# Performance work log

Hardware: AMD Instinct MI355X
Metric: run time of the kernel (lower is better)

The kernel has to match this reference:

```python
import jax, jax.numpy as jnp
import numpy as np
from jax import lax

# Orthonormal 2x2 Haar (db1). Analysis uses dwt_scale per coefficient; the
# synthesis uses 0.5*idwt_scale so that dwt_scale=0.5, idwt_scale=1.0 gives a
# perfect round trip (Hadamard matrix M, M@M = 4I, M symmetric).
DWT_SCALE = 0.5
IDWT_SCALE = 1.0
WT_LEVELS = 3
STRIDE = 1
PAD = 1  # (kernel_size - 1) // 2


def dwt2(x, s):
    # x: (B, C, H, W) -> (B, C, 4, H/2, W/2), subband order LL, LH, HL, HH
    a = x[..., 0::2, 0::2]
    b = x[..., 0::2, 1::2]
    c = x[..., 1::2, 0::2]
    d = x[..., 1::2, 1::2]
    ll = (a + b + c + d) * s
    lh = (a - b + c - d) * s
    hl = (a + b - c - d) * s
    hh = (a - b - c + d) * s
    return jnp.stack([ll, lh, hl, hh], axis=2)


def idwt2(sub, s):
    # sub: (B, C, 4, h, w) -> (B, C, 2h, 2w); inverse of dwt2 when s = 0.5/ (4*dwt_s) * ... here Hadamard symmetric
    ll, lh, hl, hh = sub[:, :, 0], sub[:, :, 1], sub[:, :, 2], sub[:, :, 3]
    a = (ll + lh + hl + hh) * s
    b = (ll - lh + hl - hh) * s
    c = (ll + lh - hl - hh) * s
    d = (ll - lh - hl + hh) * s
    B, C, h, w = a.shape
    row0 = jnp.stack([a, b], axis=-1).reshape(B, C, h, 2 * w)
    row1 = jnp.stack([c, d], axis=-1).reshape(B, C, h, 2 * w)
    return jnp.stack([row0, row1], axis=-2).reshape(B, C, 2 * h, 2 * w)


def conv2d(x, w, stride, pad):
    return lax.conv_general_dilated(
        x, w, window_strides=(stride, stride),
        padding=[(pad, pad), (pad, pad)],
        dimension_numbers=('NCHW', 'OIHW', 'NCHW'))


def wtconv_core(x, weight):
    cout4 = weight.shape[0]
    cout = cout4 // 4
    curr_ll = x
    ll_levels, high_levels = [], []
    for _ in range(WT_LEVELS):
        sub = dwt2(curr_ll, DWT_SCALE)             # (B, C, 4, h, w)
        B, C, _, h, w = sub.shape
        y = conv2d(sub.reshape(B, C * 4, h, w), weight, STRIDE, PAD)
        y = y.reshape(B, cout, 4, h, w)
        ll_levels.append(y[:, :, 0])
        high_levels.append(y[:, :, 1:])
        curr_ll = sub[:, :, 0]                     # pre-conv LL feeds next level
    next_ll = jnp.zeros_like(ll_levels[-1])
    for ll, hi in zip(reversed(ll_levels), reversed(high_levels)):
        ll = ll + next_ll
        sub = jnp.concatenate([ll[:, :, None], hi], axis=2)
        next_ll = idwt2(sub, 0.5 * IDWT_SCALE)
    return next_ll


def setup_inputs() -> dict:
    key = jax.random.key(0)
    k1, k2, k3 = jax.random.split(key, 3)
    B, C, H, W = 8, 32, 224, 224
    K = 3
    x = jax.random.normal(k1, (B, C, H, W), dtype=jnp.float32)
    fan_in = C * 4 * K * K
    bound = np.sqrt(6.0 / ((1.0 + 2.236 ** 2) * fan_in))
    weight = jax.random.uniform(k2, (C * 4, C * 4, K, K), dtype=jnp.float32,
                                minval=-bound, maxval=bound)
    bias = jax.random.normal(k3, (C,), dtype=jnp.float32) * 0.01
    return {"x": x, "weight": weight, "bias": bias}


def reference(x, weight, bias):
    H, W = x.shape[-2:]
    pad_factor = 2 ** WT_LEVELS
    pad_h = (pad_factor - H % pad_factor) % pad_factor
    pad_w = (pad_factor - W % pad_factor) % pad_factor
    xp = x
    if pad_h > 0 or pad_w > 0:
        xp = jnp.pad(x, ((0, 0), (0, 0), (0, pad_h), (0, pad_w)), mode='reflect')
    out = wtconv_core(xp, weight)
    out = out[..., :H, :W]
    return out + bias[None, :, None, None]
```

## Files before the change

kernel.cpp:

```cpp
#include <hip/hip_runtime.h>

typedef __bf16 bf16_t;
typedef __bf16 bf16x4_t __attribute__((ext_vector_type(4)));
typedef __bf16 bf16x8_t __attribute__((ext_vector_type(8)));
typedef float f32x16_t __attribute__((ext_vector_type(16)));

__device__ __forceinline__ void repack_body(const float* __restrict__ w,
                                            bf16_t* __restrict__ wt2,
                                            int o) {
  int e = o & 7;
  int lane = (o >> 3) & 63;
  int f = o >> 9;
  int wc = f & 1;
  int nt = (f >> 1) & 1;
  int kc = (f >> 2) & 3;
  int hk = (f >> 4) & 1;
  int t = f >> 5;
  int oc = wc * 64 + nt * 32 + (lane & 31);
  int ic = (hk * 8 + kc * 2 + (lane >> 5)) * 8 + e;
  wt2[o] = (bf16_t)w[((size_t)oc * 128 + ic) * 9 + t];
}

__device__ __forceinline__ void dwt_body(const float* __restrict__ in,
                                         bf16_t* __restrict__ sub,
                                         float* __restrict__ llout,
                                         int h, int w, bf16_t* lds) {
  const int bi = blockIdx.z;
  const int i = blockIdx.y;
  const int j0 = blockIdx.x * 64;
  const int tid = threadIdx.x;
  const int j = tid & 63;
  const int cg = tid >> 6;
  const int jg = j0 + j;
  const bool jok = jg < w;
  const int H2 = h * 2, W2 = w * 2;
  for (int c = cg; c < 32; c += 4) {
    float va = 0.f, vb = 0.f, vc = 0.f, vd = 0.f;
    if (jok) {
      const float2* p0 = (const float2*)(in + ((size_t)(bi * 32 + c) * H2 + 2 * i) * W2);
      const float2* p1 = (const float2*)(in + ((size_t)(bi * 32 + c) * H2 + 2 * i + 1) * W2);
      float2 r0 = p0[jg];
      float2 r1 = p1[jg];
      va = r0.x; vb = r0.y; vc = r1.x; vd = r1.y;
    }
    float ll = (va + vb + vc + vd) * 0.5f;
    float lh = (va - vb + vc - vd) * 0.5f;
    float hl = (va + vb - vc - vd) * 0.5f;
    float hh = (va - vb - vc + vd) * 0.5f;
    bf16x4_t q;
    q.x = (bf16_t)ll; q.y = (bf16_t)lh; q.z = (bf16_t)hl; q.w = (bf16_t)hh;
    *(bf16x4_t*)(&lds[j * 132 + c * 4]) = q;
    if (llout != nullptr && jok)
      llout[((size_t)(bi * 32 + c) * h + i) * w + jg] = ll;
  }
  __syncthreads();
  const size_t obase = ((size_t)bi * h + i) * w;
  for (int it = 0; it < 8; ++it) {
    int flat = it * 256 + tid;
    int jj = flat >> 5;
    int c4 = flat & 31;
    if (j0 + jj < w) {
      bf16x4_t q = *(const bf16x4_t*)(&lds[jj * 132 + c4 * 4]);
      *(bf16x4_t*)(sub + ((obase + j0 + jj) << 7) + c4 * 4) = q;
    }
  }
}

__global__ __launch_bounds__(256) void dwt0_kernel(const float* __restrict__ in,
                                                   bf16_t* __restrict__ sub,
                                                   float* __restrict__ llout,
                                                   const float* __restrict__ wsrc,
                                                   bf16_t* __restrict__ wt2,
                                                   int h, int w) {
  __shared__ __align__(16) bf16_t lds[64 * 132];
  if (blockIdx.z == 8) {
    int bid = blockIdx.y * 2 + blockIdx.x;
    for (int o = bid * 256 + threadIdx.x; o < 147456; o += 224 * 256)
      repack_body(wsrc, wt2, o);
    return;
  }
  dwt_body(in, sub, llout, h, w, lds);
}

__global__ __launch_bounds__(256) void dwt_kernel(const float* __restrict__ in,
                                                  bf16_t* __restrict__ sub,
                                                  float* __restrict__ llout,
                                                  int h, int w) {
  __shared__ __align__(16) bf16_t lds[64 * 132];
  dwt_body(in, sub, llout, h, w, lds);
}

__device__ __forceinline__ void conv_idwt_tile(
    const bf16_t* __restrict__ sub, const bf16_t* __restrict__ wt2,
    const float* __restrict__ nll, const float* __restrict__ nllup,
    const float* __restrict__ bias, float* __restrict__ out,
    int h, int w, int bi, int y0, int x0, int och, uint4* smemV) {
  char* haloS = (char*)smemV;
  float* scr = (float*)((char*)smemV + 23040);
  const int tid = threadIdx.x;
  const size_t img_base = (size_t)bi * h * w;

  const int lane = tid & 63;
  const int wav = tid >> 6;
  const int m = lane & 31;
  const int hw_ = lane >> 5;
  const int il = wav * 2 + (m >> 4);
  const int jl = m & 15;
  const int pixA = il * 18 + jl;
  const bf16_t* wlane = wt2 + (lane << 3) + (och << 9);

  f32x16_t acc[2] = {};

  for (int hk = 0; hk < 2; ++hk) {
    if (hk) __syncthreads();
    for (int it = 0; it < 6; ++it) {
      int flat = it * 256 + tid;
      int pix = flat >> 3;
      int ch = flat & 7;
      if (pix < 180) {
        int r = pix / 18;
        int c = pix - r * 18;
        int gy = y0 + r - 1;
        int gx = x0 + c - 1;
        uint4 v = make_uint4(0u, 0u, 0u, 0u);
        if ((unsigned)gy < (unsigned)h && (unsigned)gx < (unsigned)w)
          v = *(const uint4*)(sub + ((img_base + (size_t)gy * w + gx) << 7) +
                              ((hk * 8 + ch) << 3));
        *(uint4*)(haloS + (pix << 7) + ((ch ^ (pix & 7)) << 4)) = v;
      }
    }
    __syncthreads();

#pragma unroll
    for (int t = 0; t < 9; ++t) {
      const int ky = t / 3;
      const int kx = t - ky * 3;
      const bf16_t* wb = wlane + ((t * 2 + hk) << 13);
      bf16x8_t bfrag[4][2];
#pragma unroll
      for (int kc = 0; kc < 4; ++kc) {
        bfrag[kc][0] = *(const bf16x8_t*)(wb + (kc << 11));
        bfrag[kc][1] = *(const bf16x8_t*)(wb + (kc << 11) + 1024);
      }
      const int pix0 = pixA + ky * 18 + kx;
      const int s0 = pix0 & 7;
      const char* hp0 = haloS + (pix0 << 7);
#pragma unroll
      for (int kc = 0; kc < 4; ++kc) {
        const int cidx = kc * 2 + hw_;
        bf16x8_t a0 = *(const bf16x8_t*)(hp0 + ((cidx ^ s0) << 4));
        acc[0] = __builtin_amdgcn_mfma_f32_32x32x16_bf16(a0, bfrag[kc][0], acc[0], 0, 0, 0);
        acc[1] = __builtin_amdgcn_mfma_f32_32x32x16_bf16(a0, bfrag[kc][1], acc[1], 0, 0, 0);
      }
    }
  }

  const int W2 = w * 2;
  const int H2 = h * 2;
  const int hu = h >> 1, wu = w >> 1;
  const int mh_t = m >> 4;
  const int mm = m & 15;
  const int kw = mm >> 2;
  const int sw = mm & 3;

#pragma unroll
  for (int ph = 0; ph < 4; ++ph) {
    const int nt = ph >> 1;
    const int mh = ph & 1;
    if (ph) __syncthreads();
    if (mh_t == mh) {
#pragma unroll
      for (int reg = 0; reg < 16; ++reg) {
        int row = (reg & 3) + ((reg >> 2) << 3) + (hw_ << 2);
        int px = wav * 32 + row;
        scr[px * 17 + (kw << 2) + sw] = acc[nt][reg];
      }
    }
    __syncthreads();
#pragma unroll
    for (int it = 0; it < 2; ++it) {
      int idx = it * 256 + tid;
      int ox4 = idx & 7;
      int dy = (idx >> 3) & 1;
      int row = (idx >> 4) & 7;
      int k = (idx >> 7) & 3;
      int gy = y0 + row;
      int gx = x0 + ox4 * 2;
      if (gy >= h || gx >= w) continue;
      int p0 = row * 16 + ox4 * 2;
      int p1 = p0 + 1;
      float4 sa = *(const float4*)(&scr[p0 * 17 + (k << 2)]);
      float4 sb = *(const float4*)(&scr[p1 * 17 + (k << 2)]);
      float sg = dy ? -1.f : 1.f;
      float e0 = sa.x + sa.y + sg * (sa.z + sa.w);
      float e1 = sa.x - sa.y + sg * (sa.z - sa.w);
      float e2 = sb.x + sb.y + sg * (sb.z + sb.w);
      float e3 = sb.x - sb.y + sg * (sb.z - sb.w);
      int ch = och * 16 + nt * 8 + mh * 4 + k;
      float n0 = 0.f, n1 = 0.f;
      if (nll != nullptr) {
        const float* np = nll + ((size_t)(bi * 32 + ch) * h + gy) * w + gx;
        float2 nv = *(const float2*)np;
        n0 = nv.x; n1 = nv.y;
      }
      if (nllup != nullptr) {
        float u = nllup[((size_t)(bi * 32 + ch) * hu + (gy >> 1)) * wu + (gx >> 1)];
        n0 += 0.5f * u;
        n1 += 0.5f * u;
      }
      float bv = (bias != nullptr) ? bias[ch] : 0.f;
      float4 o;
      o.x = 0.5f * e0 + 0.5f * n0 + bv;
      o.y = 0.5f * e1 + 0.5f * n0 + bv;
      o.z = 0.5f * e2 + 0.5f * n1 + bv;
      o.w = 0.5f * e3 + 0.5f * n1 + bv;
      float* op = out + ((size_t)(bi * 32 + ch) * H2 + 2 * gy + dy) * W2 + 2 * gx;
      *(float4*)op = o;
    }
  }
}

__global__ __launch_bounds__(256, 4) void conv_idwt_kernel(
    const bf16_t* __restrict__ sub, const bf16_t* __restrict__ wt2,
    const float* __restrict__ nll, const float* __restrict__ nllup,
    const float* __restrict__ bias, float* __restrict__ out, int h, int w) {
  __shared__ uint4 smemV[1984];
  conv_idwt_tile(sub, wt2, nll, nllup, bias, out, h, w,
                 blockIdx.z, blockIdx.y * 8, (blockIdx.x >> 1) * 16,
                 blockIdx.x & 1, smemV);
}

__global__ __launch_bounds__(256, 4) void conv12_kernel(
    const bf16_t* __restrict__ sub1, const bf16_t* __restrict__ sub2,
    const bf16_t* __restrict__ wt2, float* __restrict__ nll1raw,
    float* __restrict__ nll2) {
  __shared__ uint4 smemV[1984];
  const int B = blockIdx.x;
  const bf16_t* sub;
  float* outp;
  int hh, bi, by, bx, och;
  if (B < 448) {
    och = B & 1;
    int q = B >> 1;
    bx = q & 3;
    int r = q >> 2;
    by = r % 7;
    bi = r / 7;
    sub = sub1; outp = nll1raw; hh = 56;
  } else {
    int lb = B - 448;
    och = lb & 1;
    int q = lb >> 1;
    bx = q & 1;
    int r = q >> 1;
    by = r & 3;
    bi = r >> 2;
    sub = sub2; outp = nll2; hh = 28;
  }
  conv_idwt_tile(sub, wt2, nullptr, nullptr, nullptr, outp, hh, hh,
                 bi, by * 8, bx * 16, och, smemV);
}

extern "C" void kernel_launch(void* const* d_in, const int* in_sizes, int n_in,
                              void* d_out, int out_size, void* d_ws, size_t ws_size,
                              hipStream_t stream) {
  if (ws_size < 66125824u) return;

  const float* x = (const float*)d_in[0];
  const float* weight = (const float*)d_in[1];
  const float* bias = (const float*)d_in[2];
  float* out = (float*)d_out;
  char* ws = (char*)d_ws;

  bf16_t* wt2 = (bf16_t*)(ws);
  bf16_t* sub0 = (bf16_t*)(ws + 294912);
  bf16_t* sub1 = (bf16_t*)(ws + 25985024);
  bf16_t* sub2 = (bf16_t*)(ws + 32407552);
  float* ll0 = (float*)(ws + 34013184);
  float* ll1 = (float*)(ws + 46858240);
  float* nll2 = (float*)(ws + 50069504);
  float* nll1 = (float*)(ws + 53280768);

  dwt0_kernel<<<dim3(2, 112, 9), 256, 0, stream>>>(x, sub0, ll0, weight, wt2, 112, 112);
  dwt_kernel<<<dim3(1, 56, 8), 256, 0, stream>>>(ll0, sub1, ll1, 56, 56);
  dwt_kernel<<<dim3(1, 28, 8), 256, 0, stream>>>(ll1, sub2, nullptr, 28, 28);
  conv12_kernel<<<576, 256, 0, stream>>>(sub1, sub2, wt2, nll1, nll2);
  conv_idwt_kernel<<<dim3(14, 14, 8), 256, 0, stream>>>(sub0, wt2, nll1, nll2, bias, out, 112, 112);
}
```

Baseline: 216.0 us.

## Retile conv so each wave owns an output-channel half over a 4x16 tile

The conv tile moves from 256 threads (8x16 pixels, with the two output-channel halves in separate blocks) to 128 threads (4x16 pixels). Each of the two waves now handles one output-channel half and two M-tiles of pixels, so one shared halo load serves all 128 output channels. This removes the duplicated halo loads across the two channel-half blocks and doubles the MFMAs per loaded weight fragment. In exchange there are more blocks, a smaller halo with proportionally more overlap rows, more accumulator registers, and occupancy set by the new launch bounds.

Result: slower. 254.9 us (+18.0%).

```diff
diff --git a/kernel.cpp b/kernel.cpp
--- a/kernel.cpp
+++ b/kernel.cpp
@@ -94,30 +94,30 @@
     const bf16_t* __restrict__ sub, const bf16_t* __restrict__ wt2,
     const float* __restrict__ nll, const float* __restrict__ nllup,
     const float* __restrict__ bias, float* __restrict__ out,
-    int h, int w, int bi, int y0, int x0, int och, uint4* smemV) {
+    int h, int w, int bi, int y0, int x0, uint4* smemV) {
   char* haloS = (char*)smemV;
-  float* scr = (float*)((char*)smemV + 23040);
+  float* scr = (float*)((char*)smemV + 13824);
   const int tid = threadIdx.x;
   const size_t img_base = (size_t)bi * h * w;
 
   const int lane = tid & 63;
-  const int wav = tid >> 6;
+  const int och = tid >> 6;
   const int m = lane & 31;
   const int hw_ = lane >> 5;
-  const int il = wav * 2 + (m >> 4);
+  const int il = m >> 4;
   const int jl = m & 15;
   const int pixA = il * 18 + jl;
   const bf16_t* wlane = wt2 + (lane << 3) + (och << 9);
 
-  f32x16_t acc[2] = {};
+  f32x16_t acc[2][2] = {};
 
   for (int hk = 0; hk < 2; ++hk) {
     if (hk) __syncthreads();
-    for (int it = 0; it < 6; ++it) {
-      int flat = it * 256 + tid;
+    for (int it = 0; it < 7; ++it) {
+      int flat = it * 128 + tid;
       int pix = flat >> 3;
       int ch = flat & 7;
-      if (pix < 180) {
+      if (pix < 108) {
         int r = pix / 18;
         int c = pix - r * 18;
         int gy = y0 + r - 1;
@@ -143,14 +143,20 @@
         bfrag[kc][1] = *(const bf16x8_t*)(wb + (kc << 11) + 1024);
       }
       const int pix0 = pixA + ky * 18 + kx;
+      const int pix1 = pix0 + 36;
       const int s0 = pix0 & 7;
+      const int s1 = pix1 & 7;
       const char* hp0 = haloS + (pix0 << 7);
+      const char* hp1 = haloS + (pix1 << 7);
 #pragma unroll
       for (int kc = 0; kc < 4; ++kc) {
         const int cidx = kc * 2 + hw_;
         bf16x8_t a0 = *(const bf16x8_t*)(hp0 + ((cidx ^ s0) << 4));
-        acc[0] = __builtin_amdgcn_mfma_f32_32x32x16_bf16(a0, bfrag[kc][0], acc[0], 0, 0, 0);
-        acc[1] = __builtin_amdgcn_mfma_f32_32x32x16_bf16(a0, bfrag[kc][1], acc[1], 0, 0, 0);
+        bf16x8_t a1 = *(const bf16x8_t*)(hp1 + ((cidx ^ s1) << 4));
+        acc[0][0] = __builtin_amdgcn_mfma_f32_32x32x16_bf16(a0, bfrag[kc][0], acc[0][0], 0, 0, 0);
+        acc[0][1] = __builtin_amdgcn_mfma_f32_32x32x16_bf16(a0, bfrag[kc][1], acc[0][1], 0, 0, 0);
+        acc[1][0] = __builtin_amdgcn_mfma_f32_32x32x16_bf16(a1, bfrag[kc][0], acc[1][0], 0, 0, 0);
+        acc[1][1] = __builtin_amdgcn_mfma_f32_32x32x16_bf16(a1, bfrag[kc][1], acc[1][1], 0, 0, 0);
       }
     }
   }
@@ -160,8 +166,6 @@
   const int hu = h >> 1, wu = w >> 1;
   const int mh_t = m >> 4;
   const int mm = m & 15;
-  const int kw = mm >> 2;
-  const int sw = mm & 3;
 
 #pragma unroll
   for (int ph = 0; ph < 4; ++ph) {
@@ -170,33 +174,36 @@
     if (ph) __syncthreads();
     if (mh_t == mh) {
 #pragma unroll
-      for (int reg = 0; reg < 16; ++reg) {
-        int row = (reg & 3) + ((reg >> 2) << 3) + (hw_ << 2);
-        int px = wav * 32 + row;
-        scr[px * 17 + (kw << 2) + sw] = acc[nt][reg];
+      for (int mt = 0; mt < 2; ++mt) {
+#pragma unroll
+        for (int reg = 0; reg < 16; ++reg) {
+          int row = (reg & 3) + ((reg >> 2) << 3) + (hw_ << 2);
+          int px = mt * 32 + row;
+          scr[px * 33 + (och << 4) + mm] = acc[mt][nt][reg];
+        }
       }
     }
     __syncthreads();
 #pragma unroll
-    for (int it = 0; it < 2; ++it) {
-      int idx = it * 256 + tid;
+    for (int it = 0; it < 4; ++it) {
+      int idx = it * 128 + tid;
       int ox4 = idx & 7;
       int dy = (idx >> 3) & 1;
-      int row = (idx >> 4) & 7;
-      int k = (idx >> 7) & 3;
+      int row = (idx >> 4) & 3;
+      int chl = idx >> 6;
       int gy = y0 + row;
       int gx = x0 + ox4 * 2;
       if (gy >= h || gx >= w) continue;
-      int p0 = row * 16 + ox4 * 2;
+      int p0 = ((row >> 1) << 5) + ((row & 1) << 4) + (ox4 << 1);
       int p1 = p0 + 1;
-      float4 sa = *(const float4*)(&scr[p0 * 17 + (k << 2)]);
-      float4 sb = *(const float4*)(&scr[p1 * 17 + (k << 2)]);
+      float4 sa = *(const float4*)(&scr[p0 * 33 + (chl << 2)]);
+      float4 sb = *(const float4*)(&scr[p1 * 33 + (chl << 2)]);
       float sg = dy ? -1.f : 1.f;
       float e0 = sa.x + sa.y + sg * (sa.z + sa.w);
       float e1 = sa.x - sa.y + sg * (sa.z - sa.w);
       float e2 = sb.x + sb.y + sg * (sb.z + sb.w);
       float e3 = sb.x - sb.y + sg * (sb.z - sb.w);
-      int ch = och * 16 + nt * 8 + mh * 4 + k;
+      int ch = ((chl >> 2) << 4) + nt * 8 + mh * 4 + (chl & 3);
       float n0 = 0.f, n1 = 0.f;
       if (nll != nullptr) {
         const float* np = nll + ((size_t)(bi * 32 + ch) * h + gy) * w + gx;
@@ -220,45 +227,40 @@
   }
 }
 
-__global__ __launch_bounds__(256, 4) void conv_idwt_kernel(
+__global__ __launch_bounds__(128, 3) void conv_idwt_kernel(
     const bf16_t* __restrict__ sub, const bf16_t* __restrict__ wt2,
     const float* __restrict__ nll, const float* __restrict__ nllup,
     const float* __restrict__ bias, float* __restrict__ out, int h, int w) {
-  __shared__ uint4 smemV[1984];
+  __shared__ uint4 smemV[1392];
   conv_idwt_tile(sub, wt2, nll, nllup, bias, out, h, w,
-                 blockIdx.z, blockIdx.y * 8, (blockIdx.x >> 1) * 16,
-                 blockIdx.x & 1, smemV);
-}
-
-__global__ __launch_bounds__(256, 4) void conv12_kernel(
+                 blockIdx.z, blockIdx.y * 4, blockIdx.x * 16, smemV);
+}
+
+__global__ __launch_bounds__(128, 3) void conv12_kernel(
     const bf16_t* __restrict__ sub1, const bf16_t* __restrict__ sub2,
     const bf16_t* __restrict__ wt2, float* __restrict__ nll1raw,
     float* __restrict__ nll2) {
-  __shared__ uint4 smemV[1984];
+  __shared__ uint4 smemV[1392];
   const int B = blockIdx.x;
   const bf16_t* sub;
   float* outp;
-  int hh, bi, by, bx, och;
+  int hh, bi, by, bx;
   if (B < 448) {
-    och = B & 1;
-    int q = B >> 1;
-    bx = q & 3;
-    int r = q >> 2;
-    by = r % 7;
-    bi = r / 7;
+    bx = B & 3;
+    int r = B >> 2;
+    by = r % 14;
+    bi = r / 14;
     sub = sub1; outp = nll1raw; hh = 56;
   } else {
     int lb = B - 448;
-    och = lb & 1;
-    int q = lb >> 1;
-    bx = q & 1;
-    int r = q >> 1;
-    by = r & 3;
-    bi = r >> 2;
+    bx = lb & 1;
+    int r = lb >> 1;
+    by = r % 7;
+    bi = r / 7;
     sub = sub2; outp = nll2; hh = 28;
   }
   conv_idwt_tile(sub, wt2, nullptr, nullptr, nullptr, outp, hh, hh,
-                 bi, by * 8, bx * 16, och, smemV);
+                 bi, by * 4, bx * 16, smemV);
 }
 
 extern "C" void kernel_launch(void* const* d_in, const int* in_sizes, int n_in,
@@ -284,6 +286,6 @@
   dwt0_kernel<<<dim3(2, 112, 9), 256, 0, stream>>>(x, sub0, ll0, weight, wt2, 112, 112);
   dwt_kernel<<<dim3(1, 56, 8), 256, 0, stream>>>(ll0, sub1, ll1, 56, 56);
   dwt_kernel<<<dim3(1, 28, 8), 256, 0, stream>>>(ll1, sub2, nullptr, 28, 28);
-  conv12_kernel<<<576, 256, 0, stream>>>(sub1, sub2, wt2, nll1, nll2);
-  conv_idwt_kernel<<<dim3(14, 14, 8), 256, 0, stream>>>(sub0, wt2, nll1, nll2, bias, out, 112, 112);
-}
+  conv12_kernel<<<560, 128, 0, stream>>>(sub1, sub2, wt2, nll1, nll2);
+  conv_idwt_kernel<<<dim3(7, 28, 8), 128, 0, stream>>>(sub0, wt2, nll1, nll2, bias, out, 112, 112);
+}
```

## Stage conv weights through double-buffered LDS via async global_load_lds

Applied to the files above, without the earlier changes.

Weight fragments were previously loaded from global memory into registers by every wave for each tap. They are now copied cooperatively into a double-buffered LDS region with global_load_lds, prefetching the next tap while the current tap's MFMAs run. This cuts redundant global weight traffic and register pressure. In exchange it adds a vmcnt drain and a block barrier per tap and grows LDS per block, which may lower occupancy.

Measured after the change: 188.0 us. -13.0%, faster.

```diff
diff --git a/kernel.cpp b/kernel.cpp
--- a/kernel.cpp
+++ b/kernel.cpp
@@ -4,6 +4,10 @@
 typedef __bf16 bf16x4_t __attribute__((ext_vector_type(4)));
 typedef __bf16 bf16x8_t __attribute__((ext_vector_type(8)));
 typedef float f32x16_t __attribute__((ext_vector_type(16)));
+
+#define AS_G(p) ((const __attribute__((address_space(1))) void*)(p))
+#define AS_L(p) ((__attribute__((address_space(3))) void*)(p))
+#define DRAIN_VM() asm volatile("s_waitcnt vmcnt(0)" ::: "memory")
 
 __device__ __forceinline__ void repack_body(const float* __restrict__ w,
                                             bf16_t* __restrict__ wt2,
@@ -96,18 +100,18 @@
     const float* __restrict__ bias, float* __restrict__ out,
     int h, int w, int bi, int y0, int x0, int och, uint4* smemV) {
   char* haloS = (char*)smemV;
+  char* Bbuf = (char*)smemV + 23040;
   float* scr = (float*)((char*)smemV + 23040);
   const int tid = threadIdx.x;
   const size_t img_base = (size_t)bi * h * w;
 
   const int lane = tid & 63;
-  const int wav = tid >> 6;
+  const int wv = tid >> 6;
   const int m = lane & 31;
   const int hw_ = lane >> 5;
-  const int il = wav * 2 + (m >> 4);
+  const int il = wv * 2 + (m >> 4);
   const int jl = m & 15;
   const int pixA = il * 18 + jl;
-  const bf16_t* wlane = wt2 + (lane << 3) + (och << 9);
 
   f32x16_t acc[2] = {};
 
@@ -129,29 +133,47 @@
         *(uint4*)(haloS + (pix << 7) + ((ch ^ (pix & 7)) << 4)) = v;
       }
     }
+    {
+      const int th0 = hk;
+#pragma unroll
+      for (int q = 0; q < 2; ++q) {
+        const bf16_t* srcp = wt2 + (((th0 << 4) + (wv << 2) + (q << 1) + och) << 9) + (lane << 3);
+        __builtin_amdgcn_global_load_lds(AS_G(srcp),
+            AS_L(Bbuf + (((wv << 1) + q) << 10)), 16, 0, 0);
+      }
+    }
+    DRAIN_VM();
     __syncthreads();
 
-#pragma unroll
+    int cur = 0;
     for (int t = 0; t < 9; ++t) {
+      if (t < 8) {
+        const int thn = ((t + 1) << 1) + hk;
+#pragma unroll
+        for (int q = 0; q < 2; ++q) {
+          const bf16_t* srcp = wt2 + (((thn << 4) + (wv << 2) + (q << 1) + och) << 9) + (lane << 3);
+          __builtin_amdgcn_global_load_lds(AS_G(srcp),
+              AS_L(Bbuf + ((cur ^ 1) << 13) + (((wv << 1) + q) << 10)), 16, 0, 0);
+        }
+      }
       const int ky = t / 3;
       const int kx = t - ky * 3;
-      const bf16_t* wb = wlane + ((t * 2 + hk) << 13);
-      bf16x8_t bfrag[4][2];
-#pragma unroll
-      for (int kc = 0; kc < 4; ++kc) {
-        bfrag[kc][0] = *(const bf16x8_t*)(wb + (kc << 11));
-        bfrag[kc][1] = *(const bf16x8_t*)(wb + (kc << 11) + 1024);
-      }
       const int pix0 = pixA + ky * 18 + kx;
       const int s0 = pix0 & 7;
       const char* hp0 = haloS + (pix0 << 7);
+      const char* bp = Bbuf + (cur << 13) + (lane << 4);
 #pragma unroll
       for (int kc = 0; kc < 4; ++kc) {
+        bf16x8_t b0 = *(const bf16x8_t*)(bp + ((kc << 1) << 10));
+        bf16x8_t b1 = *(const bf16x8_t*)(bp + (((kc << 1) + 1) << 10));
         const int cidx = kc * 2 + hw_;
         bf16x8_t a0 = *(const bf16x8_t*)(hp0 + ((cidx ^ s0) << 4));
-        acc[0] = __builtin_amdgcn_mfma_f32_32x32x16_bf16(a0, bfrag[kc][0], acc[0], 0, 0, 0);
-        acc[1] = __builtin_amdgcn_mfma_f32_32x32x16_bf16(a0, bfrag[kc][1], acc[1], 0, 0, 0);
-      }
+        acc[0] = __builtin_amdgcn_mfma_f32_32x32x16_bf16(a0, b0, acc[0], 0, 0, 0);
+        acc[1] = __builtin_amdgcn_mfma_f32_32x32x16_bf16(a0, b1, acc[1], 0, 0, 0);
+      }
+      DRAIN_VM();
+      __syncthreads();
+      cur ^= 1;
     }
   }
 
@@ -172,7 +194,7 @@
 #pragma unroll
       for (int reg = 0; reg < 16; ++reg) {
         int row = (reg & 3) + ((reg >> 2) << 3) + (hw_ << 2);
-        int px = wav * 32 + row;
+        int px = wv * 32 + row;
         scr[px * 17 + (kw << 2) + sw] = acc[nt][reg];
       }
     }
@@ -224,7 +246,7 @@
     const bf16_t* __restrict__ sub, const bf16_t* __restrict__ wt2,
     const float* __restrict__ nll, const float* __restrict__ nllup,
     const float* __restrict__ bias, float* __restrict__ out, int h, int w) {
-  __shared__ uint4 smemV[1984];
+  __shared__ uint4 smemV[2464];
   conv_idwt_tile(sub, wt2, nll, nllup, bias, out, h, w,
                  blockIdx.z, blockIdx.y * 8, (blockIdx.x >> 1) * 16,
                  blockIdx.x & 1, smemV);
@@ -234,7 +256,7 @@
     const bf16_t* __restrict__ sub1, const bf16_t* __restrict__ sub2,
     const bf16_t* __restrict__ wt2, float* __restrict__ nll1raw,
     float* __restrict__ nll2) {
-  __shared__ uint4 smemV[1984];
+  __shared__ uint4 smemV[2464];
   const int B = blockIdx.x;
   const bf16_t* sub;
   float* outp;
```
